# Performance work log

Hardware: AMD Instinct MI355X
Metric: run time of the kernel (lower is better)

## Reference

```python
import jax, jax.numpy as jnp
import numpy as np

N, E, H, L, G = 50000, 500000, 128, 4, 1000
EPS = 1e-7      # GENConv message eps
LN_EPS = 1e-5   # torch LayerNorm default


def setup_inputs() -> dict:
    key = jax.random.key(0)
    ks = jax.random.split(key, 24)
    d = {}
    d["x"] = jax.random.normal(ks[0], (N, 9), jnp.float32)
    d["edge_index"] = jax.random.randint(ks[1], (2, E), 0, N, jnp.int32)
    d["edge_attr"] = jax.random.normal(ks[2], (E, 3), jnp.float32)
    d["batch"] = jnp.sort(jax.random.randint(ks[3], (N,), 0, G, jnp.int32))
    s9, s3, sh, s2h = 1/np.sqrt(9), 1/np.sqrt(3), 1/np.sqrt(H), 1/np.sqrt(2*H)
    u = lambda k, shp, s: jax.random.uniform(k, shp, jnp.float32, -s, s)
    d["enc_node_W"] = u(ks[4], (9, H), s9)
    d["enc_node_b"] = u(ks[5], (H,), s9)
    d["enc_edge_W"] = u(ks[6], (3, H), s3)
    d["enc_edge_b"] = u(ks[7], (H,), s3)
    d["ln_g"] = jnp.ones((L, H), jnp.float32)   # DeepGCNLayer pre-norm affine
    d["ln_b"] = jnp.zeros((L, H), jnp.float32)
    d["W1"] = u(ks[8], (L, H, 2*H), sh)          # GENConv MLP layer 1
    d["b1"] = u(ks[9], (L, 2*H), sh)
    d["mlp_ln_g"] = jnp.ones((L, 2*H), jnp.float32)
    d["mlp_ln_b"] = jnp.zeros((L, 2*H), jnp.float32)
    d["W2"] = u(ks[10], (L, 2*H, H), s2h)        # GENConv MLP layer 2
    d["b2"] = u(ks[11], (L, H), s2h)
    d["t"] = jnp.ones((L,), jnp.float32)         # learnable softmax temperature, init 1.0
    return d


def layernorm(x, g, b):
    mu = x.mean(-1, keepdims=True)
    var = ((x - mu) ** 2).mean(-1, keepdims=True)
    return (x - mu) / jnp.sqrt(var + LN_EPS) * g + b


def genconv(h, src, dst, ea, t, W1, b1, lg, lb, W2, b2):
    # message: relu(x_j + edge_attr) + eps   -> [E, H]
    msg = jax.nn.relu(h[src] + ea) + EPS
    # softmax aggregation over incoming edges, per channel
    logits = t * msg
    m = jax.ops.segment_max(logits, dst, num_segments=N)
    num = jnp.exp(logits - m[dst])
    den = jax.ops.segment_sum(num, dst, num_segments=N)
    alpha = num / den[dst]
    agg = jax.ops.segment_sum(msg * alpha, dst, num_segments=N)
    out = agg + h  # root residual inside GENConv
    z = jax.nn.relu(layernorm(out @ W1 + b1, lg, lb))
    return z @ W2 + b2


def reference(x, edge_index, edge_attr, batch, enc_node_W, enc_node_b,
              enc_edge_W, enc_edge_b, ln_g, ln_b, W1, b1, mlp_ln_g, mlp_ln_b,
              W2, b2, t):
    src, dst = edge_index[0], edge_index[1]
    h = x @ enc_node_W + enc_node_b            # node encoder  [N, H]
    ea = edge_attr @ enc_edge_W + enc_edge_b   # edge encoder  [E, H]
    # layer 0: conv only (DeeperGCN forward uses layers[0].conv directly)
    h = genconv(h, src, dst, ea, t[0], W1[0], b1[0], mlp_ln_g[0], mlp_ln_b[0], W2[0], b2[0])
    # layers 1..L-1: res+ block: x + conv(relu(LN(x))); dropout is identity (eval)
    for i in range(1, L):
        z = jax.nn.relu(layernorm(h, ln_g[i], ln_b[i]))
        h = h + genconv(z, src, dst, ea, t[i], W1[i], b1[i], mlp_ln_g[i], mlp_ln_b[i], W2[i], b2[i])
    h = jax.nn.relu(layernorm(h, ln_g[0], ln_b[0]))  # reuses layer-0 norm
    # global mean pool over graphs
    counts = jax.ops.segment_sum(jnp.ones((N,), h.dtype), batch, num_segments=G)
    sums = jax.ops.segment_sum(h, batch, num_segments=G)
    return sums / jnp.maximum(counts, 1.0)[:, None]
```

## Files before the change

### kernel.cpp

```cpp
#include <hip/hip_runtime.h>

#define NN 50000
#define NE 500000
#define HD 128
#define HD2 256
#define NL 4
#define NG 1000

constexpr float MSG_EPS = 1e-7f;
constexpr float LNEPS   = 1e-5f;

typedef float  f32x4  __attribute__((ext_vector_type(4)));
typedef __bf16 bf16x8 __attribute__((ext_vector_type(8)));

__device__ __forceinline__ unsigned short f2b(float f) {
    unsigned int u = __float_as_uint(f);
    unsigned int r = u + 0x7FFFu + ((u >> 16) & 1u);
    return (unsigned short)(r >> 16);
}
__device__ __forceinline__ float b2f(unsigned short h) {
    return __uint_as_float(((unsigned int)h) << 16);
}
__device__ __forceinline__ unsigned int pack2(float a, float b) {
    return (unsigned int)f2b(a) | ((unsigned int)f2b(b) << 16);
}

__global__ void k_encode_nodes(const float* __restrict__ x, const float* __restrict__ W,
                               const float* __restrict__ b, unsigned short* __restrict__ zb) {
    int n = blockIdx.x;
    int c = threadIdx.x;
    float xr[9];
#pragma unroll
    for (int k = 0; k < 9; k++) xr[k] = x[n * 9 + k];
    float acc = b[c];
#pragma unroll
    for (int k = 0; k < 9; k++) acc = fmaf(xr[k], W[k * HD + c], acc);
    zb[n * HD + c] = f2b(acc);
}

__global__ void k_prep(const float* __restrict__ W1, const float* __restrict__ W2,
                       unsigned short* __restrict__ W1T, unsigned short* __restrict__ W2T) {
    int idx = blockIdx.x * 256 + threadIdx.x;
    {
        int k = idx & 127, n = (idx >> 7) & 255, l = idx >> 15;
        W1T[idx] = f2b(W1[(l * 128 + k) * 256 + n]);
    }
    {
        int k = idx & 255, n = (idx >> 8) & 127, l = idx >> 15;
        W2T[idx] = f2b(W2[(l * 256 + k) * 128 + n]);
    }
}

__global__ void k_hist(const int* __restrict__ dst, int* __restrict__ counts) {
    int e = blockIdx.x * blockDim.x + threadIdx.x;
    if (e < NE) atomicAdd(&counts[dst[e]], 1);
}

#define SCAN_B 512
__global__ void k_scan1(const int* __restrict__ counts, int* __restrict__ incl,
                        int* __restrict__ bsum) {
    __shared__ int s[SCAN_B];
    int i = blockIdx.x * SCAN_B + threadIdx.x;
    int v = (i < NN) ? counts[i] : 0;
    s[threadIdx.x] = v;
    __syncthreads();
    for (int off = 1; off < SCAN_B; off <<= 1) {
        int t = (threadIdx.x >= off) ? s[threadIdx.x - off] : 0;
        __syncthreads();
        s[threadIdx.x] += t;
        __syncthreads();
    }
    if (i < NN) incl[i] = s[threadIdx.x];
    if (threadIdx.x == SCAN_B - 1) bsum[blockIdx.x] = s[threadIdx.x];
}

__global__ void k_scan2(const int* __restrict__ bsum, int* __restrict__ boff, int nb) {
    __shared__ int s[128];
    int v = (threadIdx.x < nb) ? bsum[threadIdx.x] : 0;
    s[threadIdx.x] = v;
    __syncthreads();
    for (int off = 1; off < 128; off <<= 1) {
        int t = (threadIdx.x >= off) ? s[threadIdx.x - off] : 0;
        __syncthreads();
        s[threadIdx.x] += t;
        __syncthreads();
    }
    if (threadIdx.x < nb) boff[threadIdx.x] = s[threadIdx.x] - v;
}

__global__ void k_scan3(const int* __restrict__ incl, const int* __restrict__ boff,
                        int* __restrict__ row_start) {
    int i = blockIdx.x * SCAN_B + threadIdx.x;
    if (i < NN) row_start[i + 1] = incl[i] + boff[blockIdx.x];
    if (i == 0) row_start[0] = 0;
}

__global__ void k_scatter(const int* __restrict__ src, const int* __restrict__ dst,
                          const float* __restrict__ eattr, const int* __restrict__ row_start,
                          int* __restrict__ cursor, float4* __restrict__ aperm) {
    int e = blockIdx.x * blockDim.x + threadIdx.x;
    if (e >= NE) return;
    int d = dst[e];
    int p = row_start[d] + atomicAdd(&cursor[d], 1);
    float4 v;
    v.x = eattr[e * 3 + 0];
    v.y = eattr[e * 3 + 1];
    v.z = eattr[e * 3 + 2];
    v.w = __int_as_float(src[e]);
    aperm[p] = v;
}

__device__ __forceinline__ void edge_acc2(float4 a, unsigned int zz, float2 w0, float2 w1,
                                          float2 w2, float2 bb, float tv, float& num0,
                                          float& num1, float& wm0, float& wm1) {
    float zx = b2f((unsigned short)zz), zy = b2f((unsigned short)(zz >> 16));
    float eax = fmaf(a.x, w0.x, fmaf(a.y, w1.x, fmaf(a.z, w2.x, bb.x)));
    float eay = fmaf(a.x, w0.y, fmaf(a.y, w1.y, fmaf(a.z, w2.y, bb.y)));
    float mx = fmaxf(zx + eax, 0.f) + MSG_EPS;
    float my = fmaxf(zy + eay, 0.f) + MSG_EPS;
    float ex = __expf(tv * mx), ey = __expf(tv * my);
    num0 += ex;
    num1 += ey;
    wm0 = fmaf(mx, ex, wm0);
    wm1 = fmaf(my, ey, wm1);
}

__global__ __launch_bounds__(256) void k_aggregate(const unsigned short* __restrict__ zbin,
                                                   const float4* __restrict__ aperm,
                                                   const int* __restrict__ row_start,
                                                   const float* __restrict__ We,
                                                   const float* __restrict__ be,
                                                   const float* __restrict__ t, int layer,
                                                   unsigned int* __restrict__ outb) {
    int w = threadIdx.x >> 6, lane = threadIdx.x & 63;
    int n = blockIdx.x * 4 + w;
    if (n >= NN) return;
    int c = lane * 2;
    float2 w0 = *(const float2*)&We[c];
    float2 w1 = *(const float2*)&We[HD + c];
    float2 w2 = *(const float2*)&We[2 * HD + c];
    float2 bb = *(const float2*)&be[c];
    float tv = t[layer];
    int s0 = row_start[n], s1 = row_start[n + 1];
    float num0 = 0.f, num1 = 0.f, wm0 = 0.f, wm1 = 0.f;
    const unsigned int* z32 = (const unsigned int*)zbin;
    int p = s0;
    for (; p + 4 <= s1; p += 4) {
        float4 a0 = aperm[p], a1 = aperm[p + 1], a2 = aperm[p + 2], a3 = aperm[p + 3];
        unsigned int zz0 = z32[(size_t)__float_as_int(a0.w) * 64 + lane];
        unsigned int zz1 = z32[(size_t)__float_as_int(a1.w) * 64 + lane];
        unsigned int zz2 = z32[(size_t)__float_as_int(a2.w) * 64 + lane];
        unsigned int zz3 = z32[(size_t)__float_as_int(a3.w) * 64 + lane];
        edge_acc2(a0, zz0, w0, w1, w2, bb, tv, num0, num1, wm0, wm1);
        edge_acc2(a1, zz1, w0, w1, w2, bb, tv, num0, num1, wm0, wm1);
        edge_acc2(a2, zz2, w0, w1, w2, bb, tv, num0, num1, wm0, wm1);
        edge_acc2(a3, zz3, w0, w1, w2, bb, tv, num0, num1, wm0, wm1);
    }
    for (; p < s1; p++) {
        float4 a = aperm[p];
        unsigned int zz = z32[(size_t)__float_as_int(a.w) * 64 + lane];
        edge_acc2(a, zz, w0, w1, w2, bb, tv, num0, num1, wm0, wm1);
    }
    unsigned int zn = z32[(size_t)n * 64 + lane];
    float ox = ((s1 > s0) ? (wm0 / num0) : 0.f) + b2f((unsigned short)zn);
    float oy = ((s1 > s0) ? (wm1 / num1) : 0.f) + b2f((unsigned short)(zn >> 16));
    outb[(size_t)n * 64 + lane] = pack2(ox, oy);
}

#define BM 32
#define HS_LD 264
#define HT_LD 136

__global__ __launch_bounds__(256) void k_mlp(const unsigned short* __restrict__ outb,
                                             const unsigned short* __restrict__ W1T,
                                             const float* __restrict__ b1l,
                                             const float* __restrict__ lgl,
                                             const float* __restrict__ lbl,
                                             const unsigned short* __restrict__ W2T,
                                             const float* __restrict__ b2l,
                                             unsigned short* __restrict__ h,
                                             const float* __restrict__ gn,
                                             const float* __restrict__ bn,
                                             unsigned short* __restrict__ zb,
                                             int add_residual) {
    __shared__ __align__(16) unsigned short Hs[BM * HS_LD];
    __shared__ __align__(16) unsigned short Ht[BM * HT_LD];
    __shared__ __align__(16) float2 st1[2][16][4];

    int nb = blockIdx.x * BM;
    int tid = threadIdx.x;
    int w = tid >> 6, lane = tid & 63, q = lane >> 4, i = lane & 15;

    f32x4 acc[2][4];
#pragma unroll
    for (int rt = 0; rt < 2; rt++)
#pragma unroll
        for (int ct = 0; ct < 4; ct++) acc[rt][ct] = (f32x4){0.f, 0.f, 0.f, 0.f};

    bf16x8 acur[2], bcur[4];
#pragma unroll
    for (int rt = 0; rt < 2; rt++) {
        int row = nb + rt * 16 + i;
        acur[rt] = (row < NN) ? *(const bf16x8*)&outb[(size_t)row * HD + q * 8]
                              : (bf16x8)(__bf16)0.f;
    }
#pragma unroll
    for (int ct = 0; ct < 4; ct++)
        bcur[ct] = *(const bf16x8*)&W1T[(w * 64 + ct * 16 + i) * HD + q * 8];

#pragma unroll
    for (int ks = 0; ks < 4; ks++) {
        bf16x8 anxt[2], bnxt[4];
        if (ks < 3) {
#pragma unroll
            for (int rt = 0; rt < 2; rt++) {
                int row = nb + rt * 16 + i;
                anxt[rt] = (row < NN)
                               ? *(const bf16x8*)&outb[(size_t)row * HD + (ks + 1) * 32 + q * 8]
                               : (bf16x8)(__bf16)0.f;
            }
#pragma unroll
            for (int ct = 0; ct < 4; ct++)
                bnxt[ct] =
                    *(const bf16x8*)&W1T[(w * 64 + ct * 16 + i) * HD + (ks + 1) * 32 + q * 8];
        }
#pragma unroll
        for (int rt = 0; rt < 2; rt++)
#pragma unroll
            for (int ct = 0; ct < 4; ct++)
                acc[rt][ct] =
                    __builtin_amdgcn_mfma_f32_16x16x32_bf16(acur[rt], bcur[ct], acc[rt][ct],
                                                            0, 0, 0);
        if (ks < 3) {
#pragma unroll
            for (int rt = 0; rt < 2; rt++) acur[rt] = anxt[rt];
#pragma unroll
            for (int ct = 0; ct < 4; ct++) bcur[ct] = bnxt[ct];
        }
    }

#pragma unroll
    for (int ct = 0; ct < 4; ct++) {
        float bb = b1l[w * 64 + ct * 16 + i];
#pragma unroll
        for (int rt = 0; rt < 2; rt++)
#pragma unroll
            for (int r = 0; r < 4; r++) acc[rt][ct][r] += bb;
    }

    {
        float sv[2][4], qv[2][4];
#pragma unroll
        for (int rt = 0; rt < 2; rt++)
#pragma unroll
            for (int r = 0; r < 4; r++) {
                float s = acc[rt][0][r] + acc[rt][1][r] + acc[rt][2][r] + acc[rt][3][r];
                float sq = 0.f;
#pragma unroll
                for (int ct = 0; ct < 4; ct++) sq = fmaf(acc[rt][ct][r], acc[rt][ct][r], sq);
                sv[rt][r] = s;
                qv[rt][r] = sq;
            }
#pragma unroll
        for (int m = 1; m <= 8; m <<= 1)
#pragma unroll
            for (int rt = 0; rt < 2; rt++)
#pragma unroll
                for (int r = 0; r < 4; r++) {
                    sv[rt][r] += __shfl_xor(sv[rt][r], m);
                    qv[rt][r] += __shfl_xor(qv[rt][r], m);
                }
        if (i == 0) {
#pragma unroll
            for (int rt = 0; rt < 2; rt++)
#pragma unroll
                for (int r = 0; r < 4; r++)
                    st1[rt][q * 4 + r][w] = make_float2(sv[rt][r], qv[rt][r]);
        }
    }
    __syncthreads();

    {
        float mu[2][4], inv[2][4];
#pragma unroll
        for (int rt = 0; rt < 2; rt++)
#pragma unroll
            for (int r = 0; r < 4; r++) {
                const float4* sp = (const float4*)&st1[rt][q * 4 + r][0];
                float4 a = sp[0], b = sp[1];
                float S = a.x + a.z + b.x + b.z;
                float Q = a.y + a.w + b.y + b.w;
                float m_ = S * (1.f / 256.f);
                float v_ = Q * (1.f / 256.f) - m_ * m_;
                mu[rt][r] = m_;
                inv[rt][r] = rsqrtf(v_ + LNEPS);
            }
#pragma unroll
        for (int ct = 0; ct < 4; ct++) {
            float g = lgl[w * 64 + ct * 16 + i];
            float c = lbl[w * 64 + ct * 16 + i];
#pragma unroll
            for (int rt = 0; rt < 2; rt++)
#pragma unroll
                for (int r = 0; r < 4; r++) {
                    float v =
                        fmaxf(fmaf((acc[rt][ct][r] - mu[rt][r]) * inv[rt][r], g, c), 0.f);
                    Hs[(rt * 16 + q * 4 + r) * HS_LD + w * 64 + ct * 16 + i] = f2b(v);
                }
        }
    }
    __syncthreads();

    f32x4 acc2[2][2];
#pragma unroll
    for (int rt = 0; rt < 2; rt++)
#pragma unroll
        for (int ct = 0; ct < 2; ct++) acc2[rt][ct] = (f32x4){0.f, 0.f, 0.f, 0.f};

    bf16x8 hc[2], bc[2];
#pragma unroll
    for (int rt = 0; rt < 2; rt++) hc[rt] = *(const bf16x8*)&Hs[(rt * 16 + i) * HS_LD + q * 8];
#pragma unroll
    for (int ct = 0; ct < 2; ct++)
        bc[ct] = *(const bf16x8*)&W2T[(w * 32 + ct * 16 + i) * HD2 + q * 8];

#pragma unroll
    for (int ks = 0; ks < 8; ks++) {
        bf16x8 hn[2], bn2[2];
        if (ks < 7) {
#pragma unroll
            for (int rt = 0; rt < 2; rt++)
                hn[rt] = *(const bf16x8*)&Hs[(rt * 16 + i) * HS_LD + (ks + 1) * 32 + q * 8];
#pragma unroll
            for (int ct = 0; ct < 2; ct++)
                bn2[ct] =
                    *(const bf16x8*)&W2T[(w * 32 + ct * 16 + i) * HD2 + (ks + 1) * 32 + q * 8];
        }
#pragma unroll
        for (int rt = 0; rt < 2; rt++)
#pragma unroll
            for (int ct = 0; ct < 2; ct++)
                acc2[rt][ct] = __builtin_amdgcn_mfma_f32_16x16x32_bf16(hc[rt], bc[ct],
                                                                      acc2[rt][ct], 0, 0, 0);
        if (ks < 7) {
#pragma unroll
            for (int rt = 0; rt < 2; rt++) hc[rt] = hn[rt];
#pragma unroll
            for (int ct = 0; ct < 2; ct++) bc[ct] = bn2[ct];
        }
    }

#pragma unroll
    for (int ct = 0; ct < 2; ct++) {
        float bb = b2l[w * 32 + ct * 16 + i];
#pragma unroll
        for (int rt = 0; rt < 2; rt++)
#pragma unroll
            for (int r = 0; r < 4; r++)
                Ht[(rt * 16 + q * 4 + r) * HT_LD + w * 32 + ct * 16 + i] =
                    f2b(acc2[rt][ct][r] + bb);
    }
    __syncthreads();

    {
        const unsigned int* Ht32 = (const unsigned int*)Ht;
        unsigned int* h32 = (unsigned int*)h;
        unsigned int* zb32 = (unsigned int*)zb;
        float2 gg = *(const float2*)&gn[lane * 2];
        float2 cc = *(const float2*)&bn[lane * 2];
        for (int rr = w; rr < BM; rr += 4) {
            int row = nb + rr;
            if (row >= NN) break;
            unsigned int tv = Ht32[rr * (HT_LD / 2) + lane];
            float cx = b2f((unsigned short)tv), cy = b2f((unsigned short)(tv >> 16));
            if (add_residual) {
                unsigned int hv = h32[(size_t)row * 64 + lane];
                cx += b2f((unsigned short)hv);
                cy += b2f((unsigned short)(hv >> 16));
            }
            h32[(size_t)row * 64 + lane] = pack2(cx, cy);
            float s = cx + cy, sq = cx * cx + cy * cy;
#pragma unroll
            for (int m = 32; m >= 1; m >>= 1) {
                s += __shfl_xor(s, m);
                sq += __shfl_xor(sq, m);
            }
            float mu = s * (1.f / 128.f);
            float var = sq * (1.f / 128.f) - mu * mu;
            float inv = rsqrtf(var + LNEPS);
            float z0 = fmaxf(fmaf((cx - mu) * inv, gg.x, cc.x), 0.f);
            float z1 = fmaxf(fmaf((cy - mu) * inv, gg.y, cc.y), 0.f);
            zb32[(size_t)row * 64 + lane] = pack2(z0, z1);
        }
    }
}

__global__ void k_gbounds(const int* __restrict__ batch, int* __restrict__ gstart) {
    int g = blockIdx.x * blockDim.x + threadIdx.x;
    if (g > NG) return;
    int lo = 0, hi = NN;
    while (lo < hi) {
        int mid = (lo + hi) >> 1;
        if (batch[mid] < g) lo = mid + 1;
        else hi = mid;
    }
    gstart[g] = lo;
}

__global__ void k_pool(const unsigned short* __restrict__ zb, const int* __restrict__ gstart,
                       float* __restrict__ out) {
    int g = blockIdx.x;
    int c = threadIdx.x;
    int a = gstart[g], b = gstart[g + 1];
    float s0 = 0.f, s1 = 0.f;
    int n = a;
    for (; n + 2 <= b; n += 2) {
        s0 += b2f(zb[(size_t)n * HD + c]);
        s1 += b2f(zb[(size_t)(n + 1) * HD + c]);
    }
    if (n < b) s0 += b2f(zb[(size_t)n * HD + c]);
    out[g * HD + c] = (s0 + s1) / fmaxf((float)(b - a), 1.f);
}

extern "C" void kernel_launch(void* const* d_in, const int* in_sizes, int n_in, void* d_out,
                              int out_size, void* d_ws, size_t ws_size, hipStream_t stream) {
    const float* x     = (const float*)d_in[0];
    const int* ei      = (const int*)d_in[1];
    const float* eattr = (const float*)d_in[2];
    const int* batch   = (const int*)d_in[3];
    const float* encW  = (const float*)d_in[4];
    const float* encB  = (const float*)d_in[5];
    const float* eW    = (const float*)d_in[6];
    const float* eB    = (const float*)d_in[7];
    const float* ln_g  = (const float*)d_in[8];
    const float* ln_b  = (const float*)d_in[9];
    const float* W1    = (const float*)d_in[10];
    const float* b1    = (const float*)d_in[11];
    const float* mlg   = (const float*)d_in[12];
    const float* mlb   = (const float*)d_in[13];
    const float* W2    = (const float*)d_in[14];
    const float* b2    = (const float*)d_in[15];
    const float* t     = (const float*)d_in[16];
    const int* src = ei;
    const int* dst = ei + NE;

    char* w = (char*)d_ws;
    auto alloc = [&](size_t bytes) {
        char* p = w;
        w += (bytes + 255) & ~size_t(255);
        return p;
    };
    unsigned short* h    = (unsigned short*)alloc(sizeof(unsigned short) * NN * HD);
    unsigned short* zb   = (unsigned short*)alloc(sizeof(unsigned short) * NN * HD);
    unsigned int* outb   = (unsigned int*)alloc(sizeof(unsigned int) * NN * HD / 2);
    float4* aperm        = (float4*)alloc(sizeof(float4) * NE);
    int* row_start       = (int*)alloc(sizeof(int) * (NN + 1));
    int* counts          = (int*)alloc(sizeof(int) * NN);
    int* cursor          = (int*)alloc(sizeof(int) * NN);
    int* incl            = (int*)alloc(sizeof(int) * NN);
    int* bsum            = (int*)alloc(sizeof(int) * 128);
    int* boff            = (int*)alloc(sizeof(int) * 128);
    int* gstart          = (int*)alloc(sizeof(int) * (NG + 1));
    unsigned short* W1T  = (unsigned short*)alloc(sizeof(unsigned short) * NL * HD * HD2);
    unsigned short* W2T  = (unsigned short*)alloc(sizeof(unsigned short) * NL * HD2 * HD);

    hipMemsetAsync(counts, 0, sizeof(int) * NN, stream);
    hipMemsetAsync(cursor, 0, sizeof(int) * NN, stream);

    k_prep<<<512, 256, 0, stream>>>(W1, W2, W1T, W2T);
    k_encode_nodes<<<NN, HD, 0, stream>>>(x, encW, encB, zb);
    k_hist<<<(NE + 255) / 256, 256, 0, stream>>>(dst, counts);
    int nsb = (NN + SCAN_B - 1) / SCAN_B;
    k_scan1<<<nsb, SCAN_B, 0, stream>>>(counts, incl, bsum);
    k_scan2<<<1, 128, 0, stream>>>(bsum, boff, nsb);
    k_scan3<<<nsb, SCAN_B, 0, stream>>>(incl, boff, row_start);
    k_scatter<<<(NE + 255) / 256, 256, 0, stream>>>(src, dst, eattr, row_start, cursor, aperm);
    k_gbounds<<<(NG + 256) / 256, 256, 0, stream>>>(batch, gstart);

    for (int l = 0; l < NL; l++) {
        k_aggregate<<<(NN + 3) / 4, 256, 0, stream>>>(zb, aperm, row_start, eW, eB, t, l, outb);
        int ln_next = (l + 1) % NL;
        k_mlp<<<(NN + BM - 1) / BM, 256, 0, stream>>>(
            (const unsigned short*)outb, W1T + (size_t)l * HD * HD2, b1 + l * HD2,
            mlg + l * HD2, mlb + l * HD2, W2T + (size_t)l * HD2 * HD, b2 + l * HD, h,
            ln_g + ln_next * HD, ln_b + ln_next * HD, zb, l > 0);
    }
    k_pool<<<NG, HD, 0, stream>>>(zb, gstart, (float*)d_out);
}
```

Baseline: 506.1 us.

## Split aggregation edges across two waves per node and fuse setup kernels

The aggregation kernel now assigns two wavefronts to each destination node, each covering half of that node's incoming edges. The partial softmax sums are combined through shared memory, and the source index is made wave-uniform with readfirstlane. Weight prep, node encoding and the degree histogram are merged into a single setup launch, and the graph-bounds search is folded into the final scan kernel to cut launch count. The goal is more memory-level parallelism on the gather-bound aggregation and less launch overhead. The cost is a block-wide barrier, an extra shared-memory reduction, and half the waves sitting idle during the final combine.

```diff
diff --git a/kernel.cpp b/kernel.cpp
--- a/kernel.cpp
+++ b/kernel.cpp
@@ -25,38 +25,45 @@
     return (unsigned int)f2b(a) | ((unsigned int)f2b(b) << 16);
 }
 
-__global__ void k_encode_nodes(const float* __restrict__ x, const float* __restrict__ W,
-                               const float* __restrict__ b, unsigned short* __restrict__ zb) {
-    int n = blockIdx.x;
-    int c = threadIdx.x;
-    float xr[9];
-#pragma unroll
-    for (int k = 0; k < 9; k++) xr[k] = x[n * 9 + k];
-    float acc = b[c];
-#pragma unroll
-    for (int k = 0; k < 9; k++) acc = fmaf(xr[k], W[k * HD + c], acc);
-    zb[n * HD + c] = f2b(acc);
-}
-
-__global__ void k_prep(const float* __restrict__ W1, const float* __restrict__ W2,
-                       unsigned short* __restrict__ W1T, unsigned short* __restrict__ W2T) {
-    int idx = blockIdx.x * 256 + threadIdx.x;
-    {
-        int k = idx & 127, n = (idx >> 7) & 255, l = idx >> 15;
-        W1T[idx] = f2b(W1[(l * 128 + k) * 256 + n]);
-    }
-    {
-        int k = idx & 255, n = (idx >> 8) & 127, l = idx >> 15;
-        W2T[idx] = f2b(W2[(l * 256 + k) * 128 + n]);
-    }
-}
-
-__global__ void k_hist(const int* __restrict__ dst, int* __restrict__ counts) {
-    int e = blockIdx.x * blockDim.x + threadIdx.x;
-    if (e < NE) atomicAdd(&counts[dst[e]], 1);
+#define PREP_BLKS 512
+#define ENC_BLKS 25000
+#define HIST_BLKS ((NE + 255) / 256)
+
+__global__ void k_setup(const float* __restrict__ x, const float* __restrict__ encW,
+                        const float* __restrict__ encB, unsigned short* __restrict__ zb,
+                        const float* __restrict__ W1, const float* __restrict__ W2,
+                        unsigned short* __restrict__ W1T, unsigned short* __restrict__ W2T,
+                        const int* __restrict__ dst, int* __restrict__ counts) {
+    int bid = blockIdx.x, tid = threadIdx.x;
+    if (bid < PREP_BLKS) {
+        int idx = bid * 256 + tid;
+        {
+            int k = idx & 127, n = (idx >> 7) & 255, l = idx >> 15;
+            W1T[idx] = f2b(W1[(l * 128 + k) * 256 + n]);
+        }
+        {
+            int k = idx & 255, n = (idx >> 8) & 127, l = idx >> 15;
+            W2T[idx] = f2b(W2[(l * 256 + k) * 128 + n]);
+        }
+    } else if (bid < PREP_BLKS + ENC_BLKS) {
+        int n = (bid - PREP_BLKS) * 2 + (tid >> 7);
+        int c = tid & 127;
+        float xr[9];
+#pragma unroll
+        for (int k = 0; k < 9; k++) xr[k] = x[n * 9 + k];
+        float acc = encB[c];
+#pragma unroll
+        for (int k = 0; k < 9; k++) acc = fmaf(xr[k], encW[k * HD + c], acc);
+        zb[(size_t)n * HD + c] = f2b(acc);
+    } else {
+        int e = (bid - PREP_BLKS - ENC_BLKS) * 256 + tid;
+        if (e < NE) atomicAdd(&counts[dst[e]], 1);
+    }
 }
 
 #define SCAN_B 512
+#define NSB ((NN + SCAN_B - 1) / SCAN_B)
+
 __global__ void k_scan1(const int* __restrict__ counts, int* __restrict__ incl,
                         int* __restrict__ bsum) {
     __shared__ int s[SCAN_B];
@@ -88,11 +95,24 @@
     if (threadIdx.x < nb) boff[threadIdx.x] = s[threadIdx.x] - v;
 }
 
-__global__ void k_scan3(const int* __restrict__ incl, const int* __restrict__ boff,
-                        int* __restrict__ row_start) {
-    int i = blockIdx.x * SCAN_B + threadIdx.x;
-    if (i < NN) row_start[i + 1] = incl[i] + boff[blockIdx.x];
-    if (i == 0) row_start[0] = 0;
+__global__ void k_scan3g(const int* __restrict__ incl, const int* __restrict__ boff,
+                         int* __restrict__ row_start, const int* __restrict__ batch,
+                         int* __restrict__ gstart) {
+    if (blockIdx.x < NSB) {
+        int i = blockIdx.x * SCAN_B + threadIdx.x;
+        if (i < NN) row_start[i + 1] = incl[i] + boff[blockIdx.x];
+        if (i == 0) row_start[0] = 0;
+    } else {
+        int g = (blockIdx.x - NSB) * SCAN_B + threadIdx.x;
+        if (g > NG) return;
+        int lo = 0, hi = NN;
+        while (lo < hi) {
+            int mid = (lo + hi) >> 1;
+            if (batch[mid] < g) lo = mid + 1;
+            else hi = mid;
+        }
+        gstart[g] = lo;
+    }
 }
 
 __global__ void k_scatter(const int* __restrict__ src, const int* __restrict__ dst,
@@ -132,9 +152,10 @@
                                                    const float* __restrict__ be,
                                                    const float* __restrict__ t, int layer,
                                                    unsigned int* __restrict__ outb) {
+    __shared__ float4 part[4][64];
     int w = threadIdx.x >> 6, lane = threadIdx.x & 63;
-    int n = blockIdx.x * 4 + w;
-    if (n >= NN) return;
+    int n = blockIdx.x * 2 + (w >> 1);
+    int half = w & 1;
     int c = lane * 2;
     float2 w0 = *(const float2*)&We[c];
     float2 w1 = *(const float2*)&We[HD + c];
@@ -142,29 +163,45 @@
     float2 bb = *(const float2*)&be[c];
     float tv = t[layer];
     int s0 = row_start[n], s1 = row_start[n + 1];
+    int mid = s0 + ((s1 - s0 + 1) >> 1);
+    int lo = half ? mid : s0;
+    int hi = half ? s1 : mid;
     float num0 = 0.f, num1 = 0.f, wm0 = 0.f, wm1 = 0.f;
     const unsigned int* z32 = (const unsigned int*)zbin;
-    int p = s0;
-    for (; p + 4 <= s1; p += 4) {
-        float4 a0 = aperm[p], a1 = aperm[p + 1], a2 = aperm[p + 2], a3 = aperm[p + 3];
-        unsigned int zz0 = z32[(size_t)__float_as_int(a0.w) * 64 + lane];
-        unsigned int zz1 = z32[(size_t)__float_as_int(a1.w) * 64 + lane];
-        unsigned int zz2 = z32[(size_t)__float_as_int(a2.w) * 64 + lane];
-        unsigned int zz3 = z32[(size_t)__float_as_int(a3.w) * 64 + lane];
-        edge_acc2(a0, zz0, w0, w1, w2, bb, tv, num0, num1, wm0, wm1);
-        edge_acc2(a1, zz1, w0, w1, w2, bb, tv, num0, num1, wm0, wm1);
-        edge_acc2(a2, zz2, w0, w1, w2, bb, tv, num0, num1, wm0, wm1);
-        edge_acc2(a3, zz3, w0, w1, w2, bb, tv, num0, num1, wm0, wm1);
-    }
-    for (; p < s1; p++) {
+    int p = lo;
+    for (; p + 4 <= hi; p += 4) {
+        float4 A[4];
+#pragma unroll
+        for (int j = 0; j < 4; j++) A[j] = aperm[p + j];
+        unsigned int Z[4];
+#pragma unroll
+        for (int j = 0; j < 4; j++) {
+            int sj = __builtin_amdgcn_readfirstlane(__float_as_int(A[j].w));
+            Z[j] = z32[(size_t)sj * 64 + lane];
+        }
+#pragma unroll
+        for (int j = 0; j < 4; j++)
+            edge_acc2(A[j], Z[j], w0, w1, w2, bb, tv, num0, num1, wm0, wm1);
+    }
+    for (; p < hi; p++) {
         float4 a = aperm[p];
-        unsigned int zz = z32[(size_t)__float_as_int(a.w) * 64 + lane];
+        int sj = __builtin_amdgcn_readfirstlane(__float_as_int(a.w));
+        unsigned int zz = z32[(size_t)sj * 64 + lane];
         edge_acc2(a, zz, w0, w1, w2, bb, tv, num0, num1, wm0, wm1);
     }
-    unsigned int zn = z32[(size_t)n * 64 + lane];
-    float ox = ((s1 > s0) ? (wm0 / num0) : 0.f) + b2f((unsigned short)zn);
-    float oy = ((s1 > s0) ? (wm1 / num1) : 0.f) + b2f((unsigned short)(zn >> 16));
-    outb[(size_t)n * 64 + lane] = pack2(ox, oy);
+    part[w][lane] = make_float4(num0, num1, wm0, wm1);
+    __syncthreads();
+    if (half == 0) {
+        float4 a = part[w][lane];
+        float4 b = part[w + 1][lane];
+        float n0 = a.x + b.x, n1 = a.y + b.y;
+        float m0 = a.z + b.z, m1 = a.w + b.w;
+        unsigned int zn = z32[(size_t)n * 64 + lane];
+        bool has = s1 > s0;
+        float ox = (has ? (m0 / n0) : 0.f) + b2f((unsigned short)zn);
+        float oy = (has ? (m1 / n1) : 0.f) + b2f((unsigned short)(zn >> 16));
+        outb[(size_t)n * 64 + lane] = pack2(ox, oy);
+    }
 }
 
 #define BM 32
@@ -393,18 +430,6 @@
             zb32[(size_t)row * 64 + lane] = pack2(z0, z1);
         }
     }
-}
-
-__global__ void k_gbounds(const int* __restrict__ batch, int* __restrict__ gstart) {
-    int g = blockIdx.x * blockDim.x + threadIdx.x;
-    if (g > NG) return;
-    int lo = 0, hi = NN;
-    while (lo < hi) {
-        int mid = (lo + hi) >> 1;
-        if (batch[mid] < g) lo = mid + 1;
-        else hi = mid;
-    }
-    gstart[g] = lo;
 }
 
 __global__ void k_pool(const unsigned short* __restrict__ zb, const int* __restrict__ gstart,
@@ -467,18 +492,15 @@
     hipMemsetAsync(counts, 0, sizeof(int) * NN, stream);
     hipMemsetAsync(cursor, 0, sizeof(int) * NN, stream);
 
-    k_prep<<<512, 256, 0, stream>>>(W1, W2, W1T, W2T);
-    k_encode_nodes<<<NN, HD, 0, stream>>>(x, encW, encB, zb);
-    k_hist<<<(NE + 255) / 256, 256, 0, stream>>>(dst, counts);
-    int nsb = (NN + SCAN_B - 1) / SCAN_B;
-    k_scan1<<<nsb, SCAN_B, 0, stream>>>(counts, incl, bsum);
-    k_scan2<<<1, 128, 0, stream>>>(bsum, boff, nsb);
-    k_scan3<<<nsb, SCAN_B, 0, stream>>>(incl, boff, row_start);
+    k_setup<<<PREP_BLKS + ENC_BLKS + HIST_BLKS, 256, 0, stream>>>(x, encW, encB, zb, W1, W2,
+                                                                  W1T, W2T, dst, counts);
+    k_scan1<<<NSB, SCAN_B, 0, stream>>>(counts, incl, bsum);
+    k_scan2<<<1, 128, 0, stream>>>(bsum, boff, NSB);
+    k_scan3g<<<NSB + 2, SCAN_B, 0, stream>>>(incl, boff, row_start, batch, gstart);
     k_scatter<<<(NE + 255) / 256, 256, 0, stream>>>(src, dst, eattr, row_start, cursor, aperm);
-    k_gbounds<<<(NG + 256) / 256, 256, 0, stream>>>(batch, gstart);
 
     for (int l = 0; l < NL; l++) {
-        k_aggregate<<<(NN + 3) / 4, 256, 0, stream>>>(zb, aperm, row_start, eW, eB, t, l, outb);
+        k_aggregate<<<NN / 2, 256, 0, stream>>>(zb, aperm, row_start, eW, eB, t, l, outb);
         int ln_next = (l + 1) % NL;
         k_mlp<<<(NN + BM - 1) / BM, 256, 0, stream>>>(
             (const unsigned short*)outb, W1T + (size_t)l * HD * HD2, b1 + l * HD2,
```

After: 547.0 us. +8.1%, slower.
